# Kernel tuning notes

Hardware: AMD Instinct MI355X
Metric: run time of the kernel (lower is better)

Reference implementation:

```python
import jax, jax.numpy as jnp
import numpy as np

D_MODEL = 1024
NUM_HEADS = 16
HEAD_DIM = D_MODEL // NUM_HEADS
CAUSAL = True


def rope_cos_sin(seq_len, dim):
    inv_freq = 1.0 / (10000.0 ** (jnp.arange(0, dim, 2, dtype=jnp.float32) / dim))
    t = jnp.arange(seq_len, dtype=jnp.float32)
    freqs = jnp.einsum('i,j->ij', t, inv_freq)          # [S, dim/2]
    emb = jnp.concatenate([freqs, freqs], axis=-1)      # [S, dim]
    return jnp.cos(emb), jnp.sin(emb)


def rotate_half(x):
    x1, x2 = jnp.split(x, 2, axis=-1)
    return jnp.concatenate([-x2, x1], axis=-1)


def setup_inputs() -> dict:
    key = jax.random.key(0)
    k1, k2, k3, k4, k5 = jax.random.split(key, 5)
    B, S = 2, 2048
    x = jax.random.normal(k1, (B, S, D_MODEL), dtype=jnp.float32)
    s = 1.0 / np.sqrt(D_MODEL)
    W_qkv = jax.random.normal(k2, (D_MODEL, 3 * D_MODEL), dtype=jnp.float32) * s
    b_qkv = jax.random.normal(k3, (3 * D_MODEL,), dtype=jnp.float32) * 0.01
    W_out = jax.random.normal(k4, (D_MODEL, D_MODEL), dtype=jnp.float32) * s
    b_out = jax.random.normal(k5, (D_MODEL,), dtype=jnp.float32) * 0.01
    return {"x": x, "W_qkv": W_qkv, "b_qkv": b_qkv, "W_out": W_out, "b_out": b_out}


def reference(x, W_qkv, b_qkv, W_out, b_out):
    B, S, _ = x.shape
    qkv = x @ W_qkv + b_qkv                              # [B, S, 3D]
    q, k, v = jnp.split(qkv, 3, axis=-1)
    # [B, H, S, hd]
    q = q.reshape(B, S, NUM_HEADS, HEAD_DIM).transpose(0, 2, 1, 3)
    k = k.reshape(B, S, NUM_HEADS, HEAD_DIM).transpose(0, 2, 1, 3)
    v = v.reshape(B, S, NUM_HEADS, HEAD_DIM).transpose(0, 2, 1, 3)
    cos, sin = rope_cos_sin(S, HEAD_DIM)                 # [S, hd]
    cos = cos[None, None]
    sin = sin[None, None]
    q = q * cos + rotate_half(q) * sin
    k = k * cos + rotate_half(k) * sin
    scores = jnp.einsum('bhqd,bhkd->bhqk', q, k) / np.sqrt(HEAD_DIM)
    if CAUSAL:
        causal_mask = jnp.triu(jnp.ones((S, S), dtype=bool), k=1)
        scores = jnp.where(causal_mask, -jnp.inf, scores)
    attn = jax.nn.softmax(scores, axis=-1)
    out = jnp.einsum('bhqk,bhkd->bhqd', attn, v)         # [B, H, S, hd]
    out = out.transpose(0, 2, 1, 3).reshape(B, S, D_MODEL)
    return out @ W_out + b_out
```

## Files before the change

kernel.cpp:

```cpp
#include <hip/hip_runtime.h>
#include <hip/hip_bf16.h>
#include <math.h>

typedef __bf16 bf16;
typedef __bf16 bf16x8 __attribute__((ext_vector_type(8)));
typedef unsigned short ushort8 __attribute__((ext_vector_type(8)));
typedef float floatx4 __attribute__((ext_vector_type(4)));

#define MFMA_BF16(a, b, c) __builtin_amdgcn_mfma_f32_16x16x32_bf16(a, b, c, 0, 0, 0)

#define Q_SCALE 0.18033688011112042f
#define NEG_INVFREQ_LOG2 0.41524101186092029f
#define INV_2PI 0.15915494309189535f

#if __has_builtin(__builtin_amdgcn_exp2f)
#define EXP2F(x) __builtin_amdgcn_exp2f(x)
#else
#define EXP2F(x) exp2f(x)
#endif

__device__ __forceinline__ void hw_sincos_rev(float rev, float* sn, float* cs) {
#if __has_builtin(__builtin_amdgcn_sinf) && __has_builtin(__builtin_amdgcn_cosf) && \
    __has_builtin(__builtin_amdgcn_fractf)
  const float f = __builtin_amdgcn_fractf(rev);
  *sn = __builtin_amdgcn_sinf(f);
  *cs = __builtin_amdgcn_cosf(f);
#else
  sincosf(rev * 6.2831853071795864f, sn, cs);
#endif
}

__device__ __forceinline__ bf16x8 cvt8(const float4 a, const float4 b) {
  bf16x8 t;
  t[0] = (bf16)a.x; t[1] = (bf16)a.y; t[2] = (bf16)a.z; t[3] = (bf16)a.w;
  t[4] = (bf16)b.x; t[5] = (bf16)b.y; t[6] = (bf16)b.z; t[7] = (bf16)b.w;
  return t;
}

__device__ __forceinline__ unsigned int pack2(float a, float b) {
#if __has_builtin(__builtin_amdgcn_cvt_pk_bf16_f32)
  return __builtin_bit_cast(unsigned int, __builtin_amdgcn_cvt_pk_bf16_f32(a, b));
#else
  unsigned short lo = __builtin_bit_cast(unsigned short, (bf16)a);
  unsigned short hi = __builtin_bit_cast(unsigned short, (bf16)b);
  return (unsigned int)lo | ((unsigned int)hi << 16);
#endif
}

__device__ __forceinline__ void gld16(const bf16* g, bf16* l) {
  __builtin_amdgcn_global_load_lds(
      (const __attribute__((address_space(1))) unsigned int*)g,
      (__attribute__((address_space(3))) unsigned int*)l, 16, 0, 0);
}

__global__ __launch_bounds__(256) void cast_x_kernel(const float* __restrict__ in,
                                                     bf16* __restrict__ out) {
  const int i = blockIdx.x * 256 + threadIdx.x;
  const float4 a = *(const float4*)&in[(size_t)i * 8];
  const float4 b = *(const float4*)&in[(size_t)i * 8 + 4];
  *(bf16x8*)&out[(size_t)i * 8] = cvt8(a, b);
}

__global__ __launch_bounds__(256) void transpose_w_kernel(
    const float* __restrict__ in, bf16* __restrict__ out, int N, int K) {
  __shared__ __align__(16) bf16 T[64][40];
  const int t = threadIdx.x;
  const int k0 = blockIdx.y * 32, n0 = blockIdx.x * 64;
  {
    const int k = t >> 3, n8 = (t & 7) * 8;
    const float* p = &in[(size_t)(k0 + k) * N + n0 + n8];
    const float4 a = *(const float4*)p;
    const float4 b = *(const float4*)(p + 4);
    const float v[8] = {a.x, a.y, a.z, a.w, b.x, b.y, b.z, b.w};
#pragma unroll
    for (int j = 0; j < 8; j++) {
      const int n = n8 + j;
      T[n][k ^ (8 * ((n >> 3) & 3))] = (bf16)v[j];
    }
  }
  __syncthreads();
  {
    const int n = t >> 2, k8 = (t & 3) * 8;
    const int kp = k8 ^ (8 * ((n >> 3) & 3));
    *(bf16x8*)&out[(size_t)(n0 + n) * K + k0 + k8] = *(const bf16x8*)&T[n][kp];
  }
}

template <int TN, int MODE>
__global__ __launch_bounds__(256) void gemm_kernel(
    const bf16* __restrict__ A, const bf16* __restrict__ Bt,
    const float* __restrict__ bias, void* __restrict__ out0,
    bf16* __restrict__ outK, bf16* __restrict__ outV, int M, int N, int K) {
  constexpr int NI = TN / 32;
  constexpr int BI = TN / 32;
  __shared__ __align__(16) bf16 As2[2][128][32];
  __shared__ __align__(16) bf16 Bs2[2][TN][32];

  const int tid = threadIdx.x, lane = tid & 63, w = tid >> 6;
  const int c = lane & 15, quad = lane >> 4;
  const int wm = w >> 1, wn = w & 1;
  const int m0 = blockIdx.y * 128, n0 = blockIdx.x * TN;
  const int srow = lane >> 2, scol = (lane & 3) * 8;

  floatx4 acc[4][NI] = {};

  for (int k0 = 0; k0 < K; k0 += 64) {
    __syncthreads();
#pragma unroll
    for (int i = 0; i < 4; i++) {
      const int seg = w * 4 + i;
      const int kh = seg >> 3, r0 = (seg & 7) * 16;
      gld16(&A[(size_t)(m0 + r0 + srow) * K + k0 + kh * 32 + scol],
            &As2[kh][r0][0]);
    }
#pragma unroll
    for (int i = 0; i < BI; i++) {
      const int seg = w * BI + i;
      const int kh = seg / (TN / 16), r0 = (seg % (TN / 16)) * 16;
      gld16(&Bt[(size_t)(n0 + r0 + srow) * K + k0 + kh * 32 + scol],
            &Bs2[kh][r0][0]);
    }
    __syncthreads();

#pragma unroll
    for (int kh = 0; kh < 2; kh++) {
      bf16x8 af[4], bfr[NI];
#pragma unroll
      for (int mi = 0; mi < 4; mi++)
        af[mi] = *(const bf16x8*)&As2[kh][wm * 64 + mi * 16 + c][quad * 8];
#pragma unroll
      for (int ni = 0; ni < NI; ni++)
        bfr[ni] = *(const bf16x8*)&Bs2[kh][wn * (TN / 2) + ni * 16 + c][quad * 8];
#pragma unroll
      for (int mi = 0; mi < 4; mi++)
#pragma unroll
        for (int ni = 0; ni < NI; ni++)
          acc[mi][ni] = MFMA_BF16(af[mi], bfr[ni], acc[mi][ni]);
    }
  }

  if (MODE == 0) {
#pragma unroll
    for (int mi = 0; mi < 4; mi++)
#pragma unroll
      for (int ni = 0; ni < NI; ni++)
#pragma unroll
        for (int r = 0; r < 4; r++) {
          const int row = m0 + wm * 64 + mi * 16 + quad * 4 + r;
          const int col = n0 + wn * (TN / 2) + ni * 16 + c;
          ((float*)out0)[(size_t)row * N + col] = acc[mi][ni][r] + bias[col];
        }
  } else {
    const int colb = n0 + wn * (TN / 2);
    const int t = colb >> 10;
    const int h = (colb & 1023) >> 6;
    bf16* dst = (t == 0) ? (bf16*)out0 : (t == 1 ? outK : outV);
    if (t == 2) {
#pragma unroll
      for (int mi = 0; mi < 4; mi++)
#pragma unroll
        for (int ni = 0; ni < NI; ni++)
#pragma unroll
          for (int r = 0; r < 4; r++) {
            const int row = m0 + wm * 64 + mi * 16 + quad * 4 + r;
            const int col = colb + ni * 16 + c;
            const int b = row >> 11, s = row & 2047;
            dst[(((size_t)b * 16 + h) * 2048 + s) * 64 + (col & 63)] =
                (bf16)(acc[mi][ni][r] + bias[col]);
          }
    } else {
      const float qs = (t == 0) ? Q_SCALE : 1.0f;
      const float invr[2] = {exp2f(-NEG_INVFREQ_LOG2 * (float)c) * INV_2PI,
                             exp2f(-NEG_INVFREQ_LOG2 * (float)(16 + c)) * INV_2PI};
#pragma unroll
      for (int mi = 0; mi < 4; mi++) {
#pragma unroll
        for (int r = 0; r < 4; r++) {
          const int row = m0 + wm * 64 + mi * 16 + quad * 4 + r;
          const int b = row >> 11, s = row & 2047;
          const size_t base = (((size_t)b * 16 + h) * 2048 + s) * 64;
#pragma unroll
          for (int ni = 0; ni < 2; ni++) {
            float sn, cs;
            hw_sincos_rev((float)s * invr[ni], &sn, &cs);
            const float v1 = acc[mi][ni][r] + bias[colb + ni * 16 + c];
            const float v2 = acc[mi][ni + 2][r] + bias[colb + (ni + 2) * 16 + c];
            const int d = ni * 16 + c;
            dst[base + d] = (bf16)((v1 * cs - v2 * sn) * qs);
            dst[base + d + 32] = (bf16)((v2 * cs + v1 * sn) * qs);
          }
        }
      }
    }
  }
}

struct AttnState {
  floatx4 o[4];
  float l;
};

__device__ __forceinline__ void attn_step(
    const bf16x8 qf[2], const bf16x8 kf[4][2], const bf16x8 vf[4][2],
    bf16 (*PsW)[72], AttnState& st, int qglob, int kbase, bool diag, int c,
    int quad) {
  floatx4 sacc[4] = {};
#pragma unroll
  for (int kg = 0; kg < 4; kg++)
#pragma unroll
    for (int dh = 0; dh < 2; dh++)
      sacc[kg] = MFMA_BF16(kf[kg][dh], qf[dh], sacc[kg]);

#pragma unroll
  for (int kg = 0; kg < 4; kg++) {
    float p[4];
#pragma unroll
    for (int r = 0; r < 4; r++) {
      float e = EXP2F(sacc[kg][r]);
      if (diag && (kbase + kg * 16 + quad * 4 + r > qglob)) e = 0.0f;
      p[r] = e;
    }
    st.l += (p[0] + p[1]) + (p[2] + p[3]);
    const uint2 u = {pack2(p[0], p[1]), pack2(p[2], p[3])};
    *(uint2*)&PsW[c][kg * 16 + quad * 4] = u;
  }

  bf16x8 pf[2];
#pragma unroll
  for (int ks = 0; ks < 2; ks++)
    pf[ks] = *(const bf16x8*)&PsW[c][ks * 32 + quad * 8];

#pragma unroll
  for (int dg = 0; dg < 4; dg++)
#pragma unroll
    for (int ks = 0; ks < 2; ks++)
      st.o[dg] = MFMA_BF16(vf[dg][ks], pf[ks], st.o[dg]);
}

__global__ __launch_bounds__(256) void attn_kernel(const bf16* __restrict__ Q,
                                                   const bf16* __restrict__ K,
                                                   const bf16* __restrict__ V,
                                                   bf16* __restrict__ Aout) {
  const int S = 2048;
  const int bh = blockIdx.y;
  const int p = blockIdx.x;
  const int tid = threadIdx.x, lane = tid & 63, wave = tid >> 6;
  const int c = lane & 15, quad = lane >> 4;

  __shared__ __align__(16) bf16 Ks2[2][64][32];
  __shared__ __align__(16) bf16 Vt[64][72];
  __shared__ __align__(16) bf16 Ps[4][16][72];

  const bf16* Qb = Q + (size_t)bh * S * 64;
  const bf16* Kb = K + (size_t)bh * S * 64;
  const bf16* Vb = V + (size_t)bh * S * 64;
  const int b = bh >> 4, h = bh & 15;

  const int qA = p, qB = 31 - p;
  const int qgA = qA * 64 + wave * 16 + c;
  const int qgB = qB * 64 + wave * 16 + c;

  bf16x8 qfA[2], qfB[2];
#pragma unroll
  for (int dh = 0; dh < 2; dh++) {
    qfA[dh] = *(const bf16x8*)&Qb[(size_t)qgA * 64 + dh * 32 + quad * 8];
    qfB[dh] = *(const bf16x8*)&Qb[(size_t)qgB * 64 + dh * 32 + quad * 8];
  }

  AttnState stA = {}, stB = {};

  const int vcc = (tid & 7) * 8;
  const int vr2 = ((tid >> 3) + 4 * (tid & 7)) & 31;
  const int ksr = lane >> 2, ksc = (lane & 3) * 8;

  for (int kt = 0; kt <= qB; kt++) {
    __syncthreads();
#pragma unroll
    for (int i = 0; i < 2; i++) {
      const int seg = wave * 2 + i;
      const int dh = seg >> 2, r0 = (seg & 3) * 16;
      gld16(&Kb[(size_t)(kt * 64 + r0 + ksr) * 64 + dh * 32 + ksc],
            &Ks2[dh][r0][0]);
    }
    {
      const bf16* vs = &Vb[(size_t)(kt * 64 + 2 * vr2) * 64 + vcc];
      const ushort8 w0 = __builtin_bit_cast(ushort8, *(const bf16x8*)vs);
      const ushort8 w1 = __builtin_bit_cast(ushort8, *(const bf16x8*)(vs + 64));
#pragma unroll
      for (int j = 0; j < 8; j++)
        *(unsigned int*)&Vt[vcc + j][2 * vr2] =
            (unsigned int)w0[j] | ((unsigned int)w1[j] << 16);
    }
    __syncthreads();

    bf16x8 kf[4][2];
#pragma unroll
    for (int kg = 0; kg < 4; kg++)
#pragma unroll
      for (int dh = 0; dh < 2; dh++)
        kf[kg][dh] = *(const bf16x8*)&Ks2[dh][kg * 16 + c][quad * 8];

    bf16x8 vf[4][2];
#pragma unroll
    for (int dg = 0; dg < 4; dg++)
#pragma unroll
      for (int ks = 0; ks < 2; ks++)
        vf[dg][ks] = *(const bf16x8*)&Vt[dg * 16 + c][ks * 32 + quad * 8];

    attn_step(qfB, kf, vf, Ps[wave], stB, qgB, kt * 64, kt == qB, c, quad);
    if (kt <= qA)
      attn_step(qfA, kf, vf, Ps[wave], stA, qgA, kt * 64, kt == qA, c, quad);
  }

  stA.l += __shfl_xor(stA.l, 16);
  stA.l += __shfl_xor(stA.l, 32);
  stB.l += __shfl_xor(stB.l, 16);
  stB.l += __shfl_xor(stB.l, 32);
  const float ivA = 1.0f / stA.l, ivB = 1.0f / stB.l;

#pragma unroll
  for (int dg = 0; dg < 4; dg++) {
    const uint2 uA = {pack2(stA.o[dg][0] * ivA, stA.o[dg][1] * ivA),
                      pack2(stA.o[dg][2] * ivA, stA.o[dg][3] * ivA)};
    const uint2 uB = {pack2(stB.o[dg][0] * ivB, stB.o[dg][1] * ivB),
                      pack2(stB.o[dg][2] * ivB, stB.o[dg][3] * ivB)};
    *(uint2*)&Aout[((size_t)b * 2048 + qgA) * 1024 + h * 64 + dg * 16 + quad * 4] = uA;
    *(uint2*)&Aout[((size_t)b * 2048 + qgB) * 1024 + h * 64 + dg * 16 + quad * 4] = uB;
  }
}

extern "C" void kernel_launch(void* const* d_in, const int* in_sizes, int n_in,
                              void* d_out, int out_size, void* d_ws,
                              size_t ws_size, hipStream_t stream) {
  const float* x = (const float*)d_in[0];
  const float* W_qkv = (const float*)d_in[1];
  const float* b_qkv = (const float*)d_in[2];
  const float* W_out = (const float*)d_in[3];
  const float* b_out = (const float*)d_in[4];
  float* out = (float*)d_out;

  const int B = 2, S = 2048, NH = 16;
  const size_t qn = (size_t)B * NH * S * 64;

  bf16* xb = (bf16*)d_ws;
  bf16* Wqkvt = xb + qn;
  bf16* Wot = Wqkvt + 3072 * 1024;
  bf16* Qw = Wot + 1024 * 1024;
  bf16* Kw = Qw + qn;
  bf16* Vw = Kw + qn;
  bf16* AO = xb;

  cast_x_kernel<<<dim3(qn / 8 / 256), 256, 0, stream>>>(x, xb);
  transpose_w_kernel<<<dim3(3072 / 64, 1024 / 32), 256, 0, stream>>>(
      W_qkv, Wqkvt, 3072, 1024);
  transpose_w_kernel<<<dim3(1024 / 64, 1024 / 32), 256, 0, stream>>>(
      W_out, Wot, 1024, 1024);

  gemm_kernel<128, 1><<<dim3(3072 / 128, 4096 / 128), 256, 0, stream>>>(
      xb, Wqkvt, b_qkv, Qw, Kw, Vw, 4096, 3072, 1024);
  attn_kernel<<<dim3(16, B * NH), 256, 0, stream>>>(Qw, Kw, Vw, AO);
  gemm_kernel<64, 0><<<dim3(1024 / 64, 4096 / 128), 256, 0, stream>>>(
      AO, Wot, b_out, out, nullptr, nullptr, 4096, 1024, 1024);
}
```

Measured before the change: 197.1 us.

## Split attention KV loop across two partitions with merge kernel, fuse prep launches

Attention blocks now process alternating KV tiles (split by a new grid dimension), writing unnormalized fp32 partial outputs and row sums. A separate merge kernel adds the two partials, normalizes and writes bf16 in the layout the output projection expects. This doubles the number of attention blocks to improve CU occupancy and load balance. The cost is extra fp32 partial traffic and one more launch. The x cast and both weight transposes are also fused into a single prep kernel to save launches.

```diff
diff --git a/kernel.cpp b/kernel.cpp
--- a/kernel.cpp
+++ b/kernel.cpp
@@ -53,19 +53,11 @@
       (__attribute__((address_space(3))) unsigned int*)l, 16, 0, 0);
 }
 
-__global__ __launch_bounds__(256) void cast_x_kernel(const float* __restrict__ in,
-                                                     bf16* __restrict__ out) {
-  const int i = blockIdx.x * 256 + threadIdx.x;
-  const float4 a = *(const float4*)&in[(size_t)i * 8];
-  const float4 b = *(const float4*)&in[(size_t)i * 8 + 4];
-  *(bf16x8*)&out[(size_t)i * 8] = cvt8(a, b);
-}
-
-__global__ __launch_bounds__(256) void transpose_w_kernel(
-    const float* __restrict__ in, bf16* __restrict__ out, int N, int K) {
-  __shared__ __align__(16) bf16 T[64][40];
-  const int t = threadIdx.x;
-  const int k0 = blockIdx.y * 32, n0 = blockIdx.x * 64;
+__device__ __forceinline__ void transpose_tile(const float* __restrict__ in,
+                                               bf16* __restrict__ out, int N,
+                                               int bx, int by, int t,
+                                               bf16 (*T)[40]) {
+  const int k0 = by * 32, n0 = bx * 64;
   {
     const int k = t >> 3, n8 = (t & 7) * 8;
     const float* p = &in[(size_t)(k0 + k) * N + n0 + n8];
@@ -82,7 +74,27 @@
   {
     const int n = t >> 2, k8 = (t & 3) * 8;
     const int kp = k8 ^ (8 * ((n >> 3) & 3));
-    *(bf16x8*)&out[(size_t)(n0 + n) * K + k0 + k8] = *(const bf16x8*)&T[n][kp];
+    *(bf16x8*)&out[(size_t)(n0 + n) * 1024 + k0 + k8] = *(const bf16x8*)&T[n][kp];
+  }
+}
+
+__global__ __launch_bounds__(256) void prep_kernel(
+    const float* __restrict__ x, bf16* __restrict__ xb,
+    const float* __restrict__ Wq, bf16* __restrict__ Wqt,
+    const float* __restrict__ Wo, bf16* __restrict__ Wot) {
+  __shared__ __align__(16) bf16 T[64][40];
+  const int bid = blockIdx.x, t = threadIdx.x;
+  if (bid < 2048) {
+    const int i = bid * 256 + t;
+    const float4 a = *(const float4*)&x[(size_t)i * 8];
+    const float4 b = *(const float4*)&x[(size_t)i * 8 + 4];
+    *(bf16x8*)&xb[(size_t)i * 8] = cvt8(a, b);
+  } else if (bid < 3584) {
+    const int bb = bid - 2048;
+    transpose_tile(Wq, Wqt, 3072, bb % 48, bb / 48, t, T);
+  } else {
+    const int bb = bid - 3584;
+    transpose_tile(Wo, Wot, 1024, bb % 16, bb / 16, t, T);
   }
 }
 
@@ -237,13 +249,14 @@
       st.o[dg] = MFMA_BF16(vf[dg][ks], pf[ks], st.o[dg]);
 }
 
-__global__ __launch_bounds__(256) void attn_kernel(const bf16* __restrict__ Q,
-                                                   const bf16* __restrict__ K,
-                                                   const bf16* __restrict__ V,
-                                                   bf16* __restrict__ Aout) {
+__global__ __launch_bounds__(256) void attn_part_kernel(
+    const bf16* __restrict__ Q, const bf16* __restrict__ K,
+    const bf16* __restrict__ V, float* __restrict__ Opart,
+    float* __restrict__ Lpart) {
   const int S = 2048;
-  const int bh = blockIdx.y;
   const int p = blockIdx.x;
+  const int j = blockIdx.y;
+  const int bh = blockIdx.z;
   const int tid = threadIdx.x, lane = tid & 63, wave = tid >> 6;
   const int c = lane & 15, quad = lane >> 4;
 
@@ -254,7 +267,6 @@
   const bf16* Qb = Q + (size_t)bh * S * 64;
   const bf16* Kb = K + (size_t)bh * S * 64;
   const bf16* Vb = V + (size_t)bh * S * 64;
-  const int b = bh >> 4, h = bh & 15;
 
   const int qA = p, qB = 31 - p;
   const int qgA = qA * 64 + wave * 16 + c;
@@ -273,7 +285,7 @@
   const int vr2 = ((tid >> 3) + 4 * (tid & 7)) & 31;
   const int ksr = lane >> 2, ksc = (lane & 3) * 8;
 
-  for (int kt = 0; kt <= qB; kt++) {
+  for (int kt = j; kt <= qB; kt += 2) {
     __syncthreads();
 #pragma unroll
     for (int i = 0; i < 2; i++) {
@@ -287,9 +299,9 @@
       const ushort8 w0 = __builtin_bit_cast(ushort8, *(const bf16x8*)vs);
       const ushort8 w1 = __builtin_bit_cast(ushort8, *(const bf16x8*)(vs + 64));
 #pragma unroll
-      for (int j = 0; j < 8; j++)
-        *(unsigned int*)&Vt[vcc + j][2 * vr2] =
-            (unsigned int)w0[j] | ((unsigned int)w1[j] << 16);
+      for (int jj = 0; jj < 8; jj++)
+        *(unsigned int*)&Vt[vcc + jj][2 * vr2] =
+            (unsigned int)w0[jj] | ((unsigned int)w1[jj] << 16);
     }
     __syncthreads();
 
@@ -316,17 +328,36 @@
   stA.l += __shfl_xor(stA.l, 32);
   stB.l += __shfl_xor(stB.l, 16);
   stB.l += __shfl_xor(stB.l, 32);
-  const float ivA = 1.0f / stA.l, ivB = 1.0f / stB.l;
-
+
+  float* Ob = Opart + ((size_t)j * 32 + bh) * S * 64;
+  float* Lb = Lpart + ((size_t)j * 32 + bh) * S;
 #pragma unroll
   for (int dg = 0; dg < 4; dg++) {
-    const uint2 uA = {pack2(stA.o[dg][0] * ivA, stA.o[dg][1] * ivA),
-                      pack2(stA.o[dg][2] * ivA, stA.o[dg][3] * ivA)};
-    const uint2 uB = {pack2(stB.o[dg][0] * ivB, stB.o[dg][1] * ivB),
-                      pack2(stB.o[dg][2] * ivB, stB.o[dg][3] * ivB)};
-    *(uint2*)&Aout[((size_t)b * 2048 + qgA) * 1024 + h * 64 + dg * 16 + quad * 4] = uA;
-    *(uint2*)&Aout[((size_t)b * 2048 + qgB) * 1024 + h * 64 + dg * 16 + quad * 4] = uB;
-  }
+    *(floatx4*)&Ob[(size_t)qgA * 64 + dg * 16 + quad * 4] = stA.o[dg];
+    *(floatx4*)&Ob[(size_t)qgB * 64 + dg * 16 + quad * 4] = stB.o[dg];
+  }
+  if (quad == 0) {
+    Lb[qgA] = stA.l;
+    Lb[qgB] = stB.l;
+  }
+}
+
+__global__ __launch_bounds__(256) void merge_kernel(
+    const float* __restrict__ Opart, const float* __restrict__ Lpart,
+    bf16* __restrict__ AO) {
+  const int t = blockIdx.x * 256 + threadIdx.x;
+  const int d4 = t & 15;
+  const int q = (t >> 4) & 2047;
+  const int bh = t >> 15;
+  const size_t half = (size_t)32 * 2048 * 64;
+  const size_t off = ((size_t)bh * 2048 + q) * 64 + d4 * 4;
+  const float4 o0 = *(const float4*)&Opart[off];
+  const float4 o1 = *(const float4*)&Opart[half + off];
+  const float iv = 1.0f / (Lpart[bh * 2048 + q] + Lpart[32 * 2048 + bh * 2048 + q]);
+  const int b = bh >> 4, h = bh & 15;
+  const uint2 u = {pack2((o0.x + o1.x) * iv, (o0.y + o1.y) * iv),
+                   pack2((o0.z + o1.z) * iv, (o0.w + o1.w) * iv)};
+  *(uint2*)&AO[((size_t)(b * 2048 + q)) * 1024 + h * 64 + d4 * 4] = u;
 }
 
 extern "C" void kernel_launch(void* const* d_in, const int* in_sizes, int n_in,
@@ -339,8 +370,7 @@
   const float* b_out = (const float*)d_in[4];
   float* out = (float*)d_out;
 
-  const int B = 2, S = 2048, NH = 16;
-  const size_t qn = (size_t)B * NH * S * 64;
+  const size_t qn = (size_t)2 * 16 * 2048 * 64;
 
   bf16* xb = (bf16*)d_ws;
   bf16* Wqkvt = xb + qn;
@@ -348,17 +378,15 @@
   bf16* Qw = Wot + 1024 * 1024;
   bf16* Kw = Qw + qn;
   bf16* Vw = Kw + qn;
+  float* Opart = (float*)(Vw + qn);
+  float* Lpart = Opart + 2 * (size_t)32 * 2048 * 64;
   bf16* AO = xb;
 
-  cast_x_kernel<<<dim3(qn / 8 / 256), 256, 0, stream>>>(x, xb);
-  transpose_w_kernel<<<dim3(3072 / 64, 1024 / 32), 256, 0, stream>>>(
-      W_qkv, Wqkvt, 3072, 1024);
-  transpose_w_kernel<<<dim3(1024 / 64, 1024 / 32), 256, 0, stream>>>(
-      W_out, Wot, 1024, 1024);
-
+  prep_kernel<<<dim3(4096), 256, 0, stream>>>(x, xb, W_qkv, Wqkvt, W_out, Wot);
   gemm_kernel<128, 1><<<dim3(3072 / 128, 4096 / 128), 256, 0, stream>>>(
       xb, Wqkvt, b_qkv, Qw, Kw, Vw, 4096, 3072, 1024);
-  attn_kernel<<<dim3(16, B * NH), 256, 0, stream>>>(Qw, Kw, Vw, AO);
+  attn_part_kernel<<<dim3(16, 2, 32), 256, 0, stream>>>(Qw, Kw, Vw, Opart, Lpart);
+  merge_kernel<<<dim3(4096), 256, 0, stream>>>(Opart, Lpart, AO);
   gemm_kernel<64, 0><<<dim3(1024 / 64, 4096 / 128), 256, 0, stream>>>(
       AO, Wot, b_out, out, nullptr, nullptr, 4096, 1024, 1024);
 }
```

Result: slower. 204.6 us (+3.8%).
